# Kernel tuning notes

Hardware: AMD Instinct MI355X
Metric: run time of the kernel (lower is better)

The kernel has to match this reference:

```python
import jax, jax.numpy as jnp
import numpy as np

B = 16      # number of point clouds
N = 4096    # points per cloud (max segment size, static)
D = 3       # xyz


def setup_inputs() -> dict:
    key = jax.random.key(0)
    k1, k2 = jax.random.split(key)
    pred = jax.random.normal(k1, (B * N, D), dtype=jnp.float32)
    target = jax.random.normal(k2, (B * N, D), dtype=jnp.float32)
    # sorted batch assignment with equal-size segments (so N_max is static)
    batch = jnp.repeat(jnp.arange(B, dtype=jnp.int64), N)
    return {"pred": pred, "target": target, "batch": batch}


def _to_dense_batch(x, batch):
    # Faithful to torch_geometric.utils.to_dense_batch: scatter each point into
    # its (cloud, within-cloud-position) slot; padding slots stay zero.
    T = x.shape[0]
    counts = jax.ops.segment_sum(jnp.ones((T,), jnp.int32), batch, num_segments=B)
    starts = jnp.concatenate([jnp.zeros((1,), jnp.int32), jnp.cumsum(counts)[:-1]])
    pos = jnp.arange(T, dtype=jnp.int32) - starts[batch]
    dense = jnp.zeros((B, N, x.shape[1]), x.dtype).at[batch, pos].set(x)
    return dense


def _chamfer(x, y):
    # pytorch3d.loss.chamfer_distance defaults: squared L2, point_reduction="mean",
    # batch_reduction="mean"; no lengths -> padded zeros count as points (as in source).
    x2 = jnp.sum(x * x, axis=-1)                      # [B, N]
    y2 = jnp.sum(y * y, axis=-1)                      # [B, N]
    xy = jnp.einsum("bid,bjd->bij", x, y)             # [B, N, N]
    d2 = x2[:, :, None] + y2[:, None, :] - 2.0 * xy   # [B, N, N] squared dists
    cham_x = jnp.mean(jnp.min(d2, axis=2), axis=1)    # x -> nearest y, mean over points
    cham_y = jnp.mean(jnp.min(d2, axis=1), axis=1)    # y -> nearest x
    return jnp.mean(cham_x + cham_y)                  # batch mean of summed directions


def reference(pred, target, batch):
    dense_x = _to_dense_batch(pred, batch)
    dense_y = _to_dense_batch(target, batch)
    return _chamfer(dense_x, dense_y)
```

## Files before the change

kernel.cpp:

```cpp
#include <hip/hip_runtime.h>


typedef __attribute__((ext_vector_type(8))) short bf16x8;
typedef __attribute__((ext_vector_type(16))) float floatx16;

#define BB 16
#define NN 4096
#define T  256
#define NPTS (BB * NN)
#define XC 128
#define NXB (NN / XC)
#define YB 512
#define NYB (NN / YB)
#define YT 32
#define NT (YB / YT)
#define ONEBF 0x3F80u

__device__ __forceinline__ unsigned int f2bf(float f) {
    unsigned int u = __float_as_uint(f);
    u += 0x7fffu + ((u >> 16) & 1u);
    return u >> 16;
}
__device__ __forceinline__ float bf2f(unsigned int h) {
    return __uint_as_float(h << 16);
}
__device__ __forceinline__ float tree16(const floatx16& d) {
    float t0 = fminf(fminf(d[0], d[1]), d[2]);
    float t1 = fminf(fminf(d[3], d[4]), d[5]);
    float t2 = fminf(fminf(d[6], d[7]), d[8]);
    float t3 = fminf(fminf(d[9], d[10]), d[11]);
    float t4 = fminf(fminf(d[12], d[13]), d[14]);
    float u0 = fminf(fminf(t0, t1), t2);
    float u1 = fminf(fminf(t3, t4), d[15]);
    return fminf(u0, u1);
}

__global__ __launch_bounds__(T) void chamfer_prep(
    const float* __restrict__ target,
    uint4* __restrict__ rec0, uint4* __restrict__ rec1)
{
    int g = blockIdx.x * T + threadIdx.x;
    const float* yp = target + (size_t)g * 3;
    float y0 = yp[0], y1 = yp[1], y2 = yp[2];
    unsigned int h0 = f2bf(y0), h1 = f2bf(y1), h2 = f2bf(y2);
    unsigned int H0 = f2bf(-2.f * bf2f(h0));
    unsigned int H1 = f2bf(-2.f * bf2f(h1));
    unsigned int H2 = f2bf(-2.f * bf2f(h2));
    unsigned int L0 = f2bf(-2.f * (y0 - bf2f(h0)));
    unsigned int L1 = f2bf(-2.f * (y1 - bf2f(h1)));
    unsigned int L2 = f2bf(-2.f * (y2 - bf2f(h2)));
    float ysq = fmaf(y0, y0, fmaf(y1, y1, y2 * y2));
    unsigned int sh = f2bf(ysq);
    unsigned int sl = f2bf(ysq - bf2f(sh));
    rec0[g] = make_uint4(H0 | (H1 << 16), H2 | (H0 << 16),
                         H1 | (H2 << 16), L0 | (L1 << 16));
    rec1[g] = make_uint4(L2 | (ONEBF << 16), ONEBF | (sh << 16),
                         sl, 0u);
}

__global__ __launch_bounds__(T, 2) void chamfer_main(
    const float* __restrict__ pred,
    const uint4* __restrict__ rec0, const uint4* __restrict__ rec1,
    float* __restrict__ rowp,
    float* __restrict__ colf)
{
    __shared__ uint4 ldsy[2][YB];
    __shared__ float colp[4][YB];

    const int xb = blockIdx.x;
    const int b  = blockIdx.y;
    const int yb = blockIdx.z;
    const size_t ygbase = (size_t)b * NN + (size_t)yb * YB;
    const int tid  = threadIdx.x;
    const int lane = tid & 63, w = tid >> 6;
    const int kg   = lane >> 5, m = lane & 31;

    for (int i = tid; i < YB; i += T) {
        ldsy[0][i] = rec0[ygbase + i];
        ldsy[1][i] = rec1[ygbase + i];
    }

    union U { uint4 q; bf16x8 v; };
    U au;
    {
        int xi = b * NN + xb * XC + w * 32 + m;
        const float* xp = pred + (size_t)xi * 3;
        float x0 = xp[0], x1 = xp[1], x2 = xp[2];
        unsigned int h0 = f2bf(x0), h1 = f2bf(x1), h2 = f2bf(x2);
        unsigned int L0 = f2bf(x0 - bf2f(h0));
        unsigned int L1 = f2bf(x1 - bf2f(h1));
        unsigned int L2 = f2bf(x2 - bf2f(h2));
        float xsq = fmaf(x0, x0, fmaf(x1, x1, x2 * x2));
        unsigned int sh = f2bf(xsq);
        unsigned int sl = f2bf(xsq - bf2f(sh));
        au.q = make_uint4(kg ? (h2 | (sh << 16))    : (h0 | (h1 << 16)),
                          kg ? (sl | (ONEBF << 16)) : (h2 | (L0 << 16)),
                          kg ? ONEBF                : (L1 | (L2 << 16)),
                          kg ? 0u                   : (h0 | (h1 << 16)));
    }

    floatx16 acc, zacc;
#pragma unroll
    for (int r = 0; r < 16; ++r) { acc[r] = 3.402823466e38f; zacc[r] = 0.f; }
    __syncthreads();

#pragma unroll 2
    for (int t = 0; t < NT; t += 2) {
        U bu0, bu1;
        bu0.q = ldsy[kg][t * YT + m];
        bu1.q = ldsy[kg][(t + 1) * YT + m];
        floatx16 d0 = __builtin_amdgcn_mfma_f32_32x32x16_bf16(
            au.v, bu0.v, zacc, 0, 0, 0);
        floatx16 d1 = __builtin_amdgcn_mfma_f32_32x32x16_bf16(
            au.v, bu1.v, zacc, 0, 0, 0);
#pragma unroll
        for (int r = 0; r < 16; ++r)
            acc[r] = fminf(fminf(acc[r], d0[r]), d1[r]);
        float cp0 = tree16(d0);
        float cp1 = tree16(d1);
        cp0 = fminf(cp0, __shfl_xor(cp0, 32, 64));
        cp1 = fminf(cp1, __shfl_xor(cp1, 32, 64));
        if (kg == 0) {
            colp[w][t * YT + m]       = cp0;
            colp[w][(t + 1) * YT + m] = cp1;
        }
    }

    float* rowbase = rowp + ((size_t)(b * NXB + xb) * NYB + yb) * XC;
#pragma unroll
    for (int r = 0; r < 16; ++r) {
        float v = acc[r];
        v = fminf(v, __shfl_xor(v, 1, 64));
        v = fminf(v, __shfl_xor(v, 2, 64));
        v = fminf(v, __shfl_xor(v, 4, 64));
        v = fminf(v, __shfl_xor(v, 8, 64));
        v = fminf(v, __shfl_xor(v, 16, 64));
        if (m == 0) {
            int row = (r & 3) + 8 * (r >> 2) + 4 * kg;
            rowbase[w * 32 + row] = v;
        }
    }

    __syncthreads();
    float* colbase = colf + ((size_t)(b * NYB + yb) * NXB + xb) * YB;
    for (int yl = tid; yl < YB; yl += T)
        colbase[yl] = fminf(fminf(colp[0][yl], colp[1][yl]),
                            fminf(colp[2][yl], colp[3][yl]));
}

__global__ __launch_bounds__(T) void chamfer_final(
    const float* __restrict__ rowp, const float* __restrict__ colf,
    float* __restrict__ out)
{
    int e = blockIdx.x * T + threadIdx.x;
    float v = 3.402823466e38f;
    if (e < NPTS) {
        int b = e >> 12, xi = e & (NN - 1);
        int xb = xi >> 7, li = xi & (XC - 1);
        const float* p = rowp + ((size_t)(b * NXB + xb) * NYB) * XC + li;
#pragma unroll
        for (int yb = 0; yb < NYB; ++yb) v = fminf(v, p[yb * XC]);
    } else {
        int f = e - NPTS;
        int b = f >> 12, y = f & (NN - 1);
        int yb = y >> 9, yl = y & (YB - 1);
        const float* p = colf + ((size_t)(b * NYB + yb) * NXB) * YB + yl;
#pragma unroll
        for (int xb = 0; xb < NXB; ++xb) v = fminf(v, p[xb * YB]);
    }
    float s = fmaxf(v, 0.f);
#pragma unroll
    for (int off = 32; off > 0; off >>= 1)
        s += __shfl_down(s, off, 64);
    __shared__ float wsum[4];
    if ((threadIdx.x & 63) == 0) wsum[threadIdx.x >> 6] = s;
    __syncthreads();
    if (threadIdx.x == 0) {
        float t = wsum[0] + wsum[1] + wsum[2] + wsum[3];
        atomicAdd(out, t * (1.0f / (BB * NN)));
    }
}

extern "C" void kernel_launch(void* const* d_in, const int* in_sizes, int n_in,
                              void* d_out, int out_size, void* d_ws, size_t ws_size,
                              hipStream_t stream) {
    const float* pred   = (const float*)d_in[0];
    const float* target = (const float*)d_in[1];
    float* out  = (float*)d_out;
    uint4* rec0 = (uint4*)d_ws;
    uint4* rec1 = rec0 + NPTS;
    float* rowp = (float*)(rec1 + NPTS);
    float* colf = rowp + (size_t)BB * NXB * NYB * XC;

    hipMemsetAsync(out, 0, sizeof(float), stream);
    chamfer_prep<<<NPTS / T, T, 0, stream>>>(target, rec0, rec1);
    dim3 grid(NXB, BB, NYB);
    chamfer_main<<<grid, T, 0, stream>>>(pred, rec0, rec1, rowp, colf);
    chamfer_final<<<2 * NPTS / T, T, 0, stream>>>(rowp, colf, out);
}
```

Baseline: 103.1 us.

## Loop over y-chunks inside each block and write final row minima directly

```diff
diff --git a/kernel.cpp b/kernel.cpp
--- a/kernel.cpp
+++ b/kernel.cpp
@@ -10,10 +10,10 @@
 #define NPTS (BB * NN)
 #define XC 128
 #define NXB (NN / XC)
-#define YB 512
-#define NYB (NN / YB)
+#define YC 512
+#define NYB (NN / YC)
 #define YT 32
-#define NT (YB / YT)
+#define NT (YC / YT)
 #define ONEBF 0x3F80u
 
 __device__ __forceinline__ unsigned int f2bf(float f) {
@@ -61,24 +61,17 @@
 __global__ __launch_bounds__(T, 2) void chamfer_main(
     const float* __restrict__ pred,
     const uint4* __restrict__ rec0, const uint4* __restrict__ rec1,
-    float* __restrict__ rowp,
+    float* __restrict__ rowf,
     float* __restrict__ colf)
 {
-    __shared__ uint4 ldsy[2][YB];
-    __shared__ float colp[4][YB];
+    __shared__ uint4 ldsy[2][YC];
+    __shared__ float colp[4][YC];
 
     const int xb = blockIdx.x;
     const int b  = blockIdx.y;
-    const int yb = blockIdx.z;
-    const size_t ygbase = (size_t)b * NN + (size_t)yb * YB;
     const int tid  = threadIdx.x;
     const int lane = tid & 63, w = tid >> 6;
     const int kg   = lane >> 5, m = lane & 31;
-
-    for (int i = tid; i < YB; i += T) {
-        ldsy[0][i] = rec0[ygbase + i];
-        ldsy[1][i] = rec1[ygbase + i];
-    }
 
     union U { uint4 q; bf16x8 v; };
     U au;
@@ -102,31 +95,46 @@
     floatx16 acc, zacc;
 #pragma unroll
     for (int r = 0; r < 16; ++r) { acc[r] = 3.402823466e38f; zacc[r] = 0.f; }
-    __syncthreads();
+
+    for (int c = 0; c < NYB; ++c) {
+        const size_t ygbase = (size_t)b * NN + (size_t)c * YC;
+        for (int i = tid; i < YC; i += T) {
+            ldsy[0][i] = rec0[ygbase + i];
+            ldsy[1][i] = rec1[ygbase + i];
+        }
+        __syncthreads();
 
 #pragma unroll 2
-    for (int t = 0; t < NT; t += 2) {
-        U bu0, bu1;
-        bu0.q = ldsy[kg][t * YT + m];
-        bu1.q = ldsy[kg][(t + 1) * YT + m];
-        floatx16 d0 = __builtin_amdgcn_mfma_f32_32x32x16_bf16(
-            au.v, bu0.v, zacc, 0, 0, 0);
-        floatx16 d1 = __builtin_amdgcn_mfma_f32_32x32x16_bf16(
-            au.v, bu1.v, zacc, 0, 0, 0);
+        for (int t = 0; t < NT; t += 2) {
+            U bu0, bu1;
+            bu0.q = ldsy[kg][t * YT + m];
+            bu1.q = ldsy[kg][(t + 1) * YT + m];
+            floatx16 d0 = __builtin_amdgcn_mfma_f32_32x32x16_bf16(
+                au.v, bu0.v, zacc, 0, 0, 0);
+            floatx16 d1 = __builtin_amdgcn_mfma_f32_32x32x16_bf16(
+                au.v, bu1.v, zacc, 0, 0, 0);
 #pragma unroll
-        for (int r = 0; r < 16; ++r)
-            acc[r] = fminf(fminf(acc[r], d0[r]), d1[r]);
-        float cp0 = tree16(d0);
-        float cp1 = tree16(d1);
-        cp0 = fminf(cp0, __shfl_xor(cp0, 32, 64));
-        cp1 = fminf(cp1, __shfl_xor(cp1, 32, 64));
-        if (kg == 0) {
-            colp[w][t * YT + m]       = cp0;
-            colp[w][(t + 1) * YT + m] = cp1;
+            for (int r = 0; r < 16; ++r)
+                acc[r] = fminf(fminf(acc[r], d0[r]), d1[r]);
+            float cp0 = tree16(d0);
+            float cp1 = tree16(d1);
+            cp0 = fminf(cp0, __shfl_xor(cp0, 32, 64));
+            cp1 = fminf(cp1, __shfl_xor(cp1, 32, 64));
+            if (kg == 0) {
+                colp[w][t * YT + m]       = cp0;
+                colp[w][(t + 1) * YT + m] = cp1;
+            }
         }
+        __syncthreads();
+
+        float* colbase = colf + ((size_t)(b * NYB + c) * NXB + xb) * YC;
+        for (int yl = tid; yl < YC; yl += T)
+            colbase[yl] = fminf(fminf(colp[0][yl], colp[1][yl]),
+                                fminf(colp[2][yl], colp[3][yl]));
+        __syncthreads();
     }
 
-    float* rowbase = rowp + ((size_t)(b * NXB + xb) * NYB + yb) * XC;
+    float* rowbase = rowf + (size_t)b * NN + xb * XC;
 #pragma unroll
     for (int r = 0; r < 16; ++r) {
         float v = acc[r];
@@ -140,33 +148,24 @@
             rowbase[w * 32 + row] = v;
         }
     }
-
-    __syncthreads();
-    float* colbase = colf + ((size_t)(b * NYB + yb) * NXB + xb) * YB;
-    for (int yl = tid; yl < YB; yl += T)
-        colbase[yl] = fminf(fminf(colp[0][yl], colp[1][yl]),
-                            fminf(colp[2][yl], colp[3][yl]));
 }
 
 __global__ __launch_bounds__(T) void chamfer_final(
-    const float* __restrict__ rowp, const float* __restrict__ colf,
+    const float* __restrict__ rowf, const float* __restrict__ colf,
     float* __restrict__ out)
 {
     int e = blockIdx.x * T + threadIdx.x;
-    float v = 3.402823466e38f;
+    float v;
     if (e < NPTS) {
-        int b = e >> 12, xi = e & (NN - 1);
-        int xb = xi >> 7, li = xi & (XC - 1);
-        const float* p = rowp + ((size_t)(b * NXB + xb) * NYB) * XC + li;
-#pragma unroll
-        for (int yb = 0; yb < NYB; ++yb) v = fminf(v, p[yb * XC]);
+        v = rowf[e];
     } else {
         int f = e - NPTS;
         int b = f >> 12, y = f & (NN - 1);
-        int yb = y >> 9, yl = y & (YB - 1);
-        const float* p = colf + ((size_t)(b * NYB + yb) * NXB) * YB + yl;
+        int yb = y >> 9, yl = y & (YC - 1);
+        const float* p = colf + ((size_t)(b * NYB + yb) * NXB) * YC + yl;
+        v = 3.402823466e38f;
 #pragma unroll
-        for (int xb = 0; xb < NXB; ++xb) v = fminf(v, p[xb * YB]);
+        for (int xb = 0; xb < NXB; ++xb) v = fminf(v, p[xb * YC]);
     }
     float s = fmaxf(v, 0.f);
 #pragma unroll
@@ -189,12 +188,12 @@
     float* out  = (float*)d_out;
     uint4* rec0 = (uint4*)d_ws;
     uint4* rec1 = rec0 + NPTS;
-    float* rowp = (float*)(rec1 + NPTS);
-    float* colf = rowp + (size_t)BB * NXB * NYB * XC;
+    float* rowf = (float*)(rec1 + NPTS);
+    float* colf = rowf + NPTS;
 
     hipMemsetAsync(out, 0, sizeof(float), stream);
     chamfer_prep<<<NPTS / T, T, 0, stream>>>(target, rec0, rec1);
-    dim3 grid(NXB, BB, NYB);
-    chamfer_main<<<grid, T, 0, stream>>>(pred, rec0, rec1, rowp, colf);
-    chamfer_final<<<2 * NPTS / T, T, 0, stream>>>(rowp, colf, out);
+    dim3 grid(NXB, BB);
+    chamfer_main<<<grid, T, 0, stream>>>(pred, rec0, rec1, rowf, colf);
+    chamfer_final<<<2 * NPTS / T, T, 0, stream>>>(rowf, colf, out);
 }
```

After: 99.83 us. -3.2%, faster.

## Split y range in halves per block and read y records directly from global

Applied to the files above, without the earlier changes.

```diff
diff --git a/kernel.cpp b/kernel.cpp
--- a/kernel.cpp
+++ b/kernel.cpp
@@ -10,10 +10,9 @@
 #define NPTS (BB * NN)
 #define XC 128
 #define NXB (NN / XC)
-#define YB 512
-#define NYB (NN / YB)
-#define YT 32
-#define NT (YB / YT)
+#define YS 2
+#define YH (NN / YS)
+#define NTL (YH / 32)
 #define ONEBF 0x3F80u
 
 __device__ __forceinline__ unsigned int f2bf(float f) {
@@ -64,21 +63,14 @@
     float* __restrict__ rowp,
     float* __restrict__ colf)
 {
-    __shared__ uint4 ldsy[2][YB];
-    __shared__ float colp[4][YB];
+    __shared__ float colp[4][YH];
 
     const int xb = blockIdx.x;
     const int b  = blockIdx.y;
-    const int yb = blockIdx.z;
-    const size_t ygbase = (size_t)b * NN + (size_t)yb * YB;
+    const int ys = blockIdx.z;
     const int tid  = threadIdx.x;
     const int lane = tid & 63, w = tid >> 6;
     const int kg   = lane >> 5, m = lane & 31;
-
-    for (int i = tid; i < YB; i += T) {
-        ldsy[0][i] = rec0[ygbase + i];
-        ldsy[1][i] = rec1[ygbase + i];
-    }
 
     union U { uint4 q; bf16x8 v; };
     U au;
@@ -102,13 +94,15 @@
     floatx16 acc, zacc;
 #pragma unroll
     for (int r = 0; r < 16; ++r) { acc[r] = 3.402823466e38f; zacc[r] = 0.f; }
-    __syncthreads();
 
-#pragma unroll 2
-    for (int t = 0; t < NT; t += 2) {
+    const uint4* bbase = (kg ? rec1 : rec0)
+                       + (size_t)b * NN + (size_t)ys * YH + m;
+
+#pragma unroll 4
+    for (int t = 0; t < NTL; t += 2) {
         U bu0, bu1;
-        bu0.q = ldsy[kg][t * YT + m];
-        bu1.q = ldsy[kg][(t + 1) * YT + m];
+        bu0.q = bbase[(size_t)t * 32];
+        bu1.q = bbase[(size_t)(t + 1) * 32];
         floatx16 d0 = __builtin_amdgcn_mfma_f32_32x32x16_bf16(
             au.v, bu0.v, zacc, 0, 0, 0);
         floatx16 d1 = __builtin_amdgcn_mfma_f32_32x32x16_bf16(
@@ -121,12 +115,12 @@
         cp0 = fminf(cp0, __shfl_xor(cp0, 32, 64));
         cp1 = fminf(cp1, __shfl_xor(cp1, 32, 64));
         if (kg == 0) {
-            colp[w][t * YT + m]       = cp0;
-            colp[w][(t + 1) * YT + m] = cp1;
+            colp[w][t * 32 + m]       = cp0;
+            colp[w][(t + 1) * 32 + m] = cp1;
         }
     }
 
-    float* rowbase = rowp + ((size_t)(b * NXB + xb) * NYB + yb) * XC;
+    float* rowbase = rowp + ((size_t)(b * YS + ys)) * NN + xb * XC;
 #pragma unroll
     for (int r = 0; r < 16; ++r) {
         float v = acc[r];
@@ -142,8 +136,8 @@
     }
 
     __syncthreads();
-    float* colbase = colf + ((size_t)(b * NYB + yb) * NXB + xb) * YB;
-    for (int yl = tid; yl < YB; yl += T)
+    float* colbase = colf + (((size_t)(b * YS + ys)) * NXB + xb) * YH;
+    for (int yl = tid; yl < YH; yl += T)
         colbase[yl] = fminf(fminf(colp[0][yl], colp[1][yl]),
                             fminf(colp[2][yl], colp[3][yl]));
 }
@@ -153,20 +147,19 @@
     float* __restrict__ out)
 {
     int e = blockIdx.x * T + threadIdx.x;
-    float v = 3.402823466e38f;
+    float v;
     if (e < NPTS) {
-        int b = e >> 12, xi = e & (NN - 1);
-        int xb = xi >> 7, li = xi & (XC - 1);
-        const float* p = rowp + ((size_t)(b * NXB + xb) * NYB) * XC + li;
-#pragma unroll
-        for (int yb = 0; yb < NYB; ++yb) v = fminf(v, p[yb * XC]);
+        int b = e >> 12, x = e & (NN - 1);
+        v = fminf(rowp[(size_t)(b * YS) * NN + x],
+                  rowp[(size_t)(b * YS + 1) * NN + x]);
     } else {
         int f = e - NPTS;
         int b = f >> 12, y = f & (NN - 1);
-        int yb = y >> 9, yl = y & (YB - 1);
-        const float* p = colf + ((size_t)(b * NYB + yb) * NXB) * YB + yl;
+        int ys = y >> 11, yl = y & (YH - 1);
+        const float* p = colf + ((size_t)(b * YS + ys)) * NXB * YH + yl;
+        v = 3.402823466e38f;
 #pragma unroll
-        for (int xb = 0; xb < NXB; ++xb) v = fminf(v, p[xb * YB]);
+        for (int xb = 0; xb < NXB; ++xb) v = fminf(v, p[(size_t)xb * YH]);
     }
     float s = fmaxf(v, 0.f);
 #pragma unroll
@@ -190,11 +183,11 @@
     uint4* rec0 = (uint4*)d_ws;
     uint4* rec1 = rec0 + NPTS;
     float* rowp = (float*)(rec1 + NPTS);
-    float* colf = rowp + (size_t)BB * NXB * NYB * XC;
+    float* colf = rowp + (size_t)BB * YS * NN;
 
     hipMemsetAsync(out, 0, sizeof(float), stream);
     chamfer_prep<<<NPTS / T, T, 0, stream>>>(target, rec0, rec1);
-    dim3 grid(NXB, BB, NYB);
+    dim3 grid(NXB, BB, YS);
     chamfer_main<<<grid, T, 0, stream>>>(pred, rec0, rec1, rowp, colf);
     chamfer_final<<<2 * NPTS / T, T, 0, stream>>>(rowp, colf, out);
 }
```

After: 106.8 us. +3.6%, slower.
